# Performance work log

Measured on AMD Instinct MI355X. Metric: run time of the kernel, lower is better.

The kernel has to match this reference:

```python
import jax, jax.numpy as jnp
import numpy as np

K = 20
EPS = 1e-5
NEG_SLOPE = 0.2


def _graph_feature(x, k):
    # x: [B, N, C] -> edge features [B, N, k, 2C]
    xx = jnp.sum(x * x, axis=-1)                       # [B, N]
    inner = jnp.einsum('bnc,bmc->bnm', x, x)           # [B, N, N]
    neg_dist = 2.0 * inner - xx[:, :, None] - xx[:, None, :]
    idx = jax.lax.top_k(neg_dist, k)[1]                # [B, N, k] nearest neighbors
    nbr = jax.vmap(lambda f, i: f[i])(x, idx)          # [B, N, k, C]
    center = jnp.broadcast_to(x[:, :, None, :], nbr.shape)
    return jnp.concatenate([nbr - center, center], axis=-1)


def _bn(y, gamma, beta, axes):
    mu = y.mean(axes, keepdims=True)
    var = y.var(axes, keepdims=True)
    return (y - mu) * jax.lax.rsqrt(var + EPS) * gamma + beta


def _lrelu(y):
    return jnp.where(y > 0, y, NEG_SLOPE * y)


def _edge_block(feat, w, gamma, beta):
    # feat: [B, N, k, Cin], w: [Cout, Cin] (1x1 conv)
    y = jnp.einsum('bnkc,oc->bnko', feat, w)
    y = _lrelu(_bn(y, gamma, beta, (0, 1, 2)))
    return y.max(axis=2)                               # max over k -> [B, N, Cout]


def setup_inputs() -> dict:
    key = jax.random.key(0)
    ks = jax.random.split(key, 8)
    B, N = 16, 2048
    num_features = 128
    x = jax.random.normal(ks[0], (B, N, 3), dtype=jnp.float32)
    s = 0.05
    w1 = jax.random.normal(ks[1], (64, 6), dtype=jnp.float32) * s
    w2 = jax.random.normal(ks[2], (64, 128), dtype=jnp.float32) * s
    w3 = jax.random.normal(ks[3], (128, 128), dtype=jnp.float32) * s
    w4 = jax.random.normal(ks[4], (256, 256), dtype=jnp.float32) * s
    w5 = jax.random.normal(ks[5], (512, 512), dtype=jnp.float32) * s
    we = jax.random.normal(ks[6], (num_features, 512), dtype=jnp.float32) * s
    def gb(c):
        return jnp.ones((c,), jnp.float32), jnp.zeros((c,), jnp.float32)
    g1, b1 = gb(64); g2, b2 = gb(64); g3, b3 = gb(128); g4, b4 = gb(256); g5, b5 = gb(512)
    return dict(x=x, w1=w1, g1=g1, b1=b1, w2=w2, g2=g2, b2=b2, w3=w3, g3=g3, b3=b3,
                w4=w4, g4=g4, b4=b4, w5=w5, g5=g5, b5=b5, we=we)


def reference(x, w1, g1, b1, w2, g2, b2, w3, g3, b3, w4, g4, b4, w5, g5, b5, we):
    # x: [B, N, 3]
    x1 = _edge_block(_graph_feature(x, K), w1, g1, b1)    # [B, N, 64]
    x2 = _edge_block(_graph_feature(x1, K), w2, g2, b2)   # [B, N, 64]
    x3 = _edge_block(_graph_feature(x2, K), w3, g3, b3)   # [B, N, 128]
    x4 = _edge_block(_graph_feature(x3, K), w4, g4, b4)   # [B, N, 256]
    cat = jnp.concatenate([x1, x2, x3, x4], axis=-1)      # [B, N, 512]
    y = jnp.einsum('bnc,oc->bno', cat, w5)                # conv5 (1x1 conv1d)
    y = _lrelu(_bn(y, g5, b5, (0, 1)))
    y = y.max(axis=1)                                     # global max pool -> [B, 512]
    return y @ we.T                                       # embedding -> [B, num_features]
```

## Files before the change

### kernel.cpp

```cpp
#include <hip/hip_runtime.h>
#include <hip/hip_bf16.h>
#include <cstdint>

#define B_ 16
#define N_ 2048
#define KNN_K 20
#define EPS_ 1e-5f
#define SLOPE_ 0.2f
#define IMS 4.8828125e-4f

typedef __attribute__((ext_vector_type(4))) float f32x4;
typedef __attribute__((ext_vector_type(8))) short bf16x8;
typedef __attribute__((ext_vector_type(8))) _Float16 f16x8;

static __device__ __forceinline__ float lrelu(float v){ return v > 0.f ? v : SLOPE_*v; }

static __device__ __forceinline__ unsigned encf(float f){
  unsigned b = __float_as_uint(f);
  return (b & 0x80000000u) ? ~b : (b | 0x80000000u);
}
static __device__ __forceinline__ float decf(unsigned u){
  unsigned b = (u & 0x80000000u) ? (u ^ 0x80000000u) : ~u;
  return __uint_as_float(b);
}
static __device__ __forceinline__ short bfbits(float v){
  __hip_bfloat16 h = __float2bfloat16(v);
  return *reinterpret_cast<short*>(&h);
}
static __device__ __forceinline__ short h16(float v){
  _Float16 h = (_Float16)v;
  return *reinterpret_cast<short*>(&h);
}
static __device__ __forceinline__ float h2f(short s){
  _Float16 h = *reinterpret_cast<_Float16*>(&s);
  return (float)h;
}

template<int C, int CP>
__global__ __launch_bounds__(256) void convert_kernel(const float* __restrict__ f, int lda,
                                                      short* __restrict__ fbf, size_t plane,
                                                      float* __restrict__ xx){
  int wid  = (blockIdx.x * 256 + threadIdx.x) >> 6;
  int lane = threadIdx.x & 63;
  if (wid >= B_*N_) return;
  const float* p = f + (size_t)wid*lda;
  float s = 0.f;
  for (int c = lane; c < CP; c += 64){
    float v = (c < C) ? p[c] : 0.f;
    short h = h16(v);
    short m = h16((v - h2f(h)) * 2048.f);
    size_t o = (size_t)wid*CP + c;
    fbf[o] = h;
    fbf[plane + o] = m;
    s += v*v;
  }
  #pragma unroll
  for (int off=32; off; off>>=1) s += __shfl_down(s, off);
  if (lane==0) xx[wid] = s;
}

template<int CP>
__global__ __launch_bounds__(256, 2) void knn_mfma(const short* __restrict__ fbf, size_t plane,
                                                const float* __restrict__ xx,
                                                float* __restrict__ pval, int* __restrict__ pidx){
  constexpr int SP = CP + 8;
  constexpr int CH = CP/8;
  constexpr int KC = CP/32;
  constexpr int PFH = CP/32;
  constexpr int FMBS = 2*64*SP;
  __shared__ __align__(16) short fmb[FMBS];
  __shared__ float dtile[64*65];
  __shared__ float xn_s[64], xm_s[64];

  int b   = blockIdx.x >> 6;
  int rem = blockIdx.x & 63;
  int n0  = (rem >> 1) << 6;
  int mh  = rem & 1;
  int mbase = mh << 10;
  int tid = threadIdx.x;
  int w    = tid >> 6;
  int lane = tid & 63;
  int fr = lane & 15, hi = lane >> 4;
  int r_loc = lane >> 2, csub = lane & 3;
  int gb = lane & 60;
  int myrow = w*16 + r_loc;
  size_t browoff = (size_t)b * N_;

  f16x8 aH[KC], aM[KC];
  {
    size_t arow = (browoff + n0 + w*16 + fr) * (size_t)CP;
    #pragma unroll
    for (int kc=0; kc<KC; ++kc){
      aH[kc] = *(const f16x8*)&fbf[arow + kc*32 + hi*8];
      aM[kc] = *(const f16x8*)&fbf[plane + arow + kc*32 + hi*8];
    }
  }
  if (tid < 64) xn_s[tid] = xx[browoff + n0 + tid];

  float sv[5]; int si[5];
  #pragma unroll
  for (int j=0;j<5;++j){ sv[j] = -1e30f; si[j] = 0x7FFFFFFF; }

  f16x8 pf[PFH];
  float xmreg = 0.f;
  auto PFLOAD = [&](int mt){
    int m0 = mbase + (mt<<6);
    #pragma unroll
    for (int j=0;j<PFH;++j){
      int i = tid + j*256;
      int r = i/CH, cq = i - r*CH;
      pf[j] = *(const f16x8*)&fbf[(browoff + m0 + r)*(size_t)CP + cq*8];
    }
    if (tid < 64) xmreg = xx[browoff + m0 + tid];
  };
  auto WRITEPF = [&](int mt){
    int m0 = mbase + (mt<<6);
    #pragma unroll
    for (int j=0;j<PFH;++j){
      int i = tid + j*256;
      int r = i/CH, cq = i - r*CH;
      *(f16x8*)&fmb[r*SP + cq*8] = pf[j];
    }
    #pragma unroll
    for (int j=0;j<PFH;++j){
      int i = tid + j*256;
      int r = i/CH, cq = i - r*CH;
      f16x8 v = *(const f16x8*)&fbf[plane + (browoff + m0 + r)*(size_t)CP + cq*8];
      *(f16x8*)&fmb[64*SP + r*SP + cq*8] = v;
    }
    if (tid < 64) xm_s[tid] = xmreg;
  };

  PFLOAD(0);
  WRITEPF(0);
  __syncthreads();

  for (int mt = 0; mt < 16; ++mt){
    int m0 = mbase + (mt << 6);
    if (mt + 1 < 16) PFLOAD(mt + 1);

    f32x4 accH[4], accM[4];
    #pragma unroll
    for (int ct=0; ct<4; ++ct){ accH[ct] = (f32x4){0.f,0.f,0.f,0.f}; accM[ct] = accH[ct]; }
    const short* BH = fmb;
    const short* BM = fmb + 64*SP;
    #pragma unroll
    for (int kc = 0; kc < KC; ++kc){
      #pragma unroll
      for (int ct=0; ct<4; ++ct){
        int boff = (ct*16 + fr)*SP + kc*32 + hi*8;
        f16x8 bh = *(const f16x8*)&BH[boff];
        f16x8 bm = *(const f16x8*)&BM[boff];
        accH[ct] = __builtin_amdgcn_mfma_f32_16x16x32_f16(aH[kc], bh, accH[ct], 0,0,0);
        accM[ct] = __builtin_amdgcn_mfma_f32_16x16x32_f16(aM[kc], bh, accM[ct], 0,0,0);
        accM[ct] = __builtin_amdgcn_mfma_f32_16x16x32_f16(aH[kc], bm, accM[ct], 0,0,0);
      }
    }
    __syncthreads();

    #pragma unroll
    for (int reg=0; reg<4; ++reg){
      int nl = w*16 + hi*4 + reg;
      float xn = xn_s[nl];
      #pragma unroll
      for (int ct=0; ct<4; ++ct)
        dtile[nl*65 + ct*16 + fr] = 2.f*(accH[ct][reg] + IMS*accM[ct][reg]) - xn - xm_s[ct*16 + fr];
    }

    int base = myrow*65 + csub*16;
    float thr = __shfl(sv[4], lane | 3);
    unsigned qm = 0u;
    #pragma unroll
    for (int jj=0; jj<16; ++jj){
      float v = dtile[base + jj];
      qm |= (v > thr) ? (1u << jj) : 0u;
    }
    unsigned long long bal = __ballot(qm != 0u);
    while (bal){
      unsigned nib = (unsigned)((bal >> gb) & 0xFull);
      int leader = nib ? (gb + (int)__builtin_ctz(nib)) : 64;
      int bbit = (int)__builtin_ctz(qm | 0x10000u);
      float mv = dtile[base + (bbit & 15)];
      int mid = m0 + (csub << 4) + bbit;
      float cv = __shfl(mv, leader);
      int   cid = __shfl(mid, leader);
      qm = (lane == leader) ? (qm & (qm - 1u)) : qm;
      int cnt = 0;
      #pragma unroll
      for (int j=0;j<5;++j) cnt += (sv[j] >= cv) ? 1 : 0;
      cnt += __shfl_xor(cnt, 1);
      cnt += __shfl_xor(cnt, 2);
      int pos = nib ? cnt : 20;
      float pv = __shfl_up(sv[4], 1);
      int   pi = __shfl_up(si[4], 1);
      #pragma unroll
      for (int j=0;j<5;++j){
        int g = csub*5 + j;
        float ns = (g < pos) ? sv[j] : ((g == pos) ? cv : pv);
        int   ni = (g < pos) ? si[j] : ((g == pos) ? cid : pi);
        pv = sv[j]; pi = si[j];
        sv[j] = ns; si[j] = ni;
      }
      bal = __ballot(qm != 0u);
    }

    if (mt + 1 < 16){
      WRITEPF(mt + 1);
      __syncthreads();
    }
  }

  size_t orow = browoff + n0 + myrow;
  float* pvo = pval + (orow*2 + mh)*KNN_K + csub*5;
  int*   pio = pidx + (orow*2 + mh)*KNN_K + csub*5;
  #pragma unroll
  for (int j=0;j<5;++j){ pvo[j] = sv[j]; pio[j] = si[j]; }
}

__global__ __launch_bounds__(256) void knn_merge(const float* __restrict__ pval,
                                                 const int* __restrict__ pidx,
                                                 int* __restrict__ idxout){
  int r = blockIdx.x*256 + threadIdx.x;
  if (r >= B_*N_) return;
  const float* va = pval + (size_t)r*2*KNN_K;
  const float* vb = va + KNN_K;
  const int*   ia = pidx + (size_t)r*2*KNN_K;
  const int*   ib = ia + KNN_K;
  int i=0, j=0;
  #pragma unroll
  for (int t=0;t<KNN_K;++t){
    float a = va[i], bq = vb[j];
    bool ta = (a >= bq);
    idxout[(size_t)r*KNN_K + t] = ta ? ia[i] : ib[j];
    i += ta ? 1 : 0; j += ta ? 0 : 1;
  }
}

template<int CP>
__global__ __launch_bounds__(256) void gemm_pq2(const short* __restrict__ fbf, size_t plane,
                                                const float* __restrict__ Wsrc, int Cin,
                                                float* __restrict__ P, float* __restrict__ Qo, int O){
  constexpr int BK = (CP < 64) ? CP : 64;
  constexpr int SP = BK + 8;
  __shared__ short Ah[64*SP];
  __shared__ short Am[64*SP];
  __shared__ short WAh[64*SP];
  __shared__ short WAm[64*SP];
  __shared__ short WQh[64*SP];
  __shared__ short WQm[64*SP];
  int obl = O >> 6;
  int bo = ((int)blockIdx.x % obl) << 6;
  int bm = ((int)blockIdx.x / obl) << 6;
  int tid = threadIdx.x;
  int w = tid >> 6, lane = tid & 63;
  int fr = lane & 15, hi = lane >> 4;
  f32x4 aPH[4], aPM[4], aQH[4], aQM[4];
  #pragma unroll
  for (int ct=0; ct<4; ++ct){
    aPH[ct] = (f32x4){0.f,0.f,0.f,0.f};
    aPM[ct] = aPH[ct]; aQH[ct] = aPH[ct]; aQM[ct] = aPH[ct];
  }

  for (int k0=0; k0<CP; k0+=BK){
    __syncthreads();
    for (int i=tid; i < 64*(BK/8); i += 256){
      int r = i/(BK/8), cq = i%(BK/8);
      size_t src = ((size_t)bm + r)*CP + k0 + cq*8;
      *(f16x8*)&Ah[r*SP + cq*8] = *(const f16x8*)&fbf[src];
      *(f16x8*)&Am[r*SP + cq*8] = *(const f16x8*)&fbf[plane + src];
    }
    for (int i=tid; i < 64*(BK/8); i += 256){
      int r = i/(BK/8), cq = i%(BK/8);
      f16x8 vah, vam, vqh, vqm;
      #pragma unroll
      for (int e=0;e<8;++e){
        int c = k0 + cq*8 + e;
        float wa = 0.f, wqv = 0.f;
        if (c < Cin){
          wa  = Wsrc[(size_t)(bo + r)*2*Cin + c];
          wqv = Wsrc[(size_t)(bo + r)*2*Cin + Cin + c] - wa;
        }
        _Float16 ha = (_Float16)wa;
        vah[e] = ha;
        vam[e] = (_Float16)((wa - (float)ha) * 2048.f);
        _Float16 hq = (_Float16)wqv;
        vqh[e] = hq;
        vqm[e] = (_Float16)((wqv - (float)hq) * 2048.f);
      }
      *(f16x8*)&WAh[r*SP + cq*8] = vah;
      *(f16x8*)&WAm[r*SP + cq*8] = vam;
      *(f16x8*)&WQh[r*SP + cq*8] = vqh;
      *(f16x8*)&WQm[r*SP + cq*8] = vqm;
    }
    __syncthreads();
    #pragma unroll
    for (int kc=0; kc<BK/32; ++kc){
      f16x8 ah = *(const f16x8*)&Ah[(w*16 + fr)*SP + kc*32 + hi*8];
      f16x8 am = *(const f16x8*)&Am[(w*16 + fr)*SP + kc*32 + hi*8];
      #pragma unroll
      for (int ct=0; ct<4; ++ct){
        int boff = (ct*16 + fr)*SP + kc*32 + hi*8;
        f16x8 bh = *(const f16x8*)&WAh[boff];
        f16x8 bm = *(const f16x8*)&WAm[boff];
        f16x8 qh = *(const f16x8*)&WQh[boff];
        f16x8 qm = *(const f16x8*)&WQm[boff];
        aPH[ct] = __builtin_amdgcn_mfma_f32_16x16x32_f16(ah, bh, aPH[ct], 0,0,0);
        aPM[ct] = __builtin_amdgcn_mfma_f32_16x16x32_f16(am, bh, aPM[ct], 0,0,0);
        aPM[ct] = __builtin_amdgcn_mfma_f32_16x16x32_f16(ah, bm, aPM[ct], 0,0,0);
        aQH[ct] = __builtin_amdgcn_mfma_f32_16x16x32_f16(ah, qh, aQH[ct], 0,0,0);
        aQM[ct] = __builtin_amdgcn_mfma_f32_16x16x32_f16(am, qh, aQM[ct], 0,0,0);
        aQM[ct] = __builtin_amdgcn_mfma_f32_16x16x32_f16(ah, qm, aQM[ct], 0,0,0);
      }
    }
  }
  #pragma unroll
  for (int ct=0; ct<4; ++ct)
    #pragma unroll
    for (int reg=0; reg<4; ++reg){
      int row = bm + w*16 + hi*4 + reg;
      size_t o = (size_t)row*O + bo + ct*16 + fr;
      P[o]  = aPH[ct][reg] + IMS*aPM[ct][reg];
      Qo[o] = aQH[ct][reg] + IMS*aQM[ct][reg];
    }
}

__global__ __launch_bounds__(256) void gemm_bf16_stats(const float* __restrict__ A,
                                                       const float* __restrict__ Wt,
                                                       const float* __restrict__ g5,
                                                       float* __restrict__ sums,
                                                       float* __restrict__ sumsq,
                                                       unsigned* __restrict__ maxenc){
  __shared__ short As[128*72];
  __shared__ short Bs[64*72];
  __shared__ float s1[64], s2[64];
  int bm = (int)(blockIdx.x >> 3) << 7;
  int bo = (int)(blockIdx.x & 7) << 6;
  int tid = threadIdx.x;
  int w = tid >> 6, lane = tid & 63;
  int fr = lane & 15, hi = lane >> 4;
  f32x4 acc[2][4];
  #pragma unroll
  for (int g=0; g<2; ++g)
    #pragma unroll
    for (int ct=0; ct<4; ++ct) acc[g][ct] = (f32x4){0.f,0.f,0.f,0.f};

  for (int k0=0; k0<512; k0+=64){
    __syncthreads();
    #pragma unroll 2
    for (int i = tid; i < 1024; i += 256){
      int r = i >> 3, cq = i & 7;
      const float* src = &A[(size_t)(bm + r)*512 + k0 + cq*8];
      bf16x8 v;
      #pragma unroll
      for (int e=0;e<8;++e) v[e] = bfbits(src[e]);
      *(bf16x8*)&As[r*72 + cq*8] = v;
    }
    #pragma unroll 2
    for (int i = tid; i < 512; i += 256){
      int r = i >> 3, cq = i & 7;
      const float* src = &Wt[(size_t)(bo + r)*512 + k0 + cq*8];
      bf16x8 v;
      #pragma unroll
      for (int e=0;e<8;++e) v[e] = bfbits(src[e]);
      *(bf16x8*)&Bs[r*72 + cq*8] = v;
    }
    __syncthreads();
    #pragma unroll
    for (int kc=0; kc<2; ++kc){
      bf16x8 a0 = *(const bf16x8*)&As[(w*32 +      fr)*72 + kc*32 + hi*8];
      bf16x8 a1 = *(const bf16x8*)&As[(w*32 + 16 + fr)*72 + kc*32 + hi*8];
      #pragma unroll
      for (int ct=0; ct<4; ++ct){
        bf16x8 bb = *(const bf16x8*)&Bs[(ct*16 + fr)*72 + kc*32 + hi*8];
        acc[0][ct] = __builtin_amdgcn_mfma_f32_16x16x32_bf16(a0, bb, acc[0][ct], 0,0,0);
        acc[1][ct] = __builtin_amdgcn_mfma_f32_16x16x32_bf16(a1, bb, acc[1][ct], 0,0,0);
      }
    }
  }

  __syncthreads();
  if (tid < 64){ s1[tid] = 0.f; s2[tid] = 0.f; }
  __syncthreads();
  int bidx = bm >> 11;
  #pragma unroll
  for (int ct=0; ct<4; ++ct){
    int o = bo + ct*16 + fr;
    float ga = g5[o];
    float s = 0.f, ss = 0.f, mx = -1e30f;
    #pragma unroll
    for (int g=0; g<2; ++g)
      #pragma unroll
      for (int reg=0; reg<4; ++reg){
        float v = acc[g][ct][reg];
        s += v; ss += v*v;
        float sel = ga >= 0.f ? v : -v;
        mx = fmaxf(mx, sel);
      }
    s  += __shfl_xor(s, 16);  s  += __shfl_xor(s, 32);
    ss += __shfl_xor(ss, 16); ss += __shfl_xor(ss, 32);
    mx = fmaxf(mx, __shfl_xor(mx, 16)); mx = fmaxf(mx, __shfl_xor(mx, 32));
    if (hi == 0){
      atomicAdd(&s1[ct*16 + fr], s);
      atomicAdd(&s2[ct*16 + fr], ss);
      atomicMax(&maxenc[bidx*512 + o], encf(mx));
    }
  }
  __syncthreads();
  if (tid < 64){
    atomicAdd(&sums[bo + tid],  s1[tid]);
    atomicAdd(&sumsq[bo + tid], s2[tid]);
  }
}

__global__ void zero_f_kernel(float* p, int n){
  int i = blockIdx.x*blockDim.x + threadIdx.x;
  if (i < n) p[i] = 0.f;
}
__global__ void zero_u_kernel(unsigned* p, int n){
  int i = blockIdx.x*blockDim.x + threadIdx.x;
  if (i < n) p[i] = 0u;
}

__global__ __launch_bounds__(256) void edge_agg(const float* __restrict__ P, const float* __restrict__ Q,
      const int* __restrict__ idx, const float* __restrict__ gamma,
      float* __restrict__ S, float* __restrict__ sums, float* __restrict__ sumsq, int O){
  const int ROWS = 64;
  int rpi = 256 / O;
  int iters = ROWS / rpi;
  int row0 = blockIdx.x * ROWS;
  int tid = threadIdx.x;
  int o  = tid % O;
  int rl = tid / O;
  int b  = row0 / N_;
  __shared__ int sidx[4][KNN_K];
  __shared__ float s1[256], s2[256];
  float g = gamma[o];
  float csum=0.f, csumsq=0.f;
  for (int it=0; it<iters; ++it){
    __syncthreads();
    if (tid < KNN_K*rpi) sidx[tid/KNN_K][tid%KNN_K] = idx[(size_t)(row0 + it*rpi)*KNN_K + tid];
    __syncthreads();
    int row = row0 + it*rpi + rl;
    float q = Q[(size_t)row*O + o];
    float mx=-1e30f, mn=1e30f, s=0.f, ss=0.f;
    #pragma unroll
    for (int k=0;k<KNN_K;++k){
      int m = sidx[rl][k];
      float p = P[((size_t)b*N_ + m)*O + o];
      mx = fmaxf(mx,p); mn = fminf(mn,p);
      float y = p + q; s += y; ss += y*y;
    }
    csum += s; csumsq += ss;
    S[(size_t)row*O + o] = (g >= 0.f ? mx : mn) + q;
  }
  s1[tid]=0.f; s2[tid]=0.f;
  __syncthreads();
  atomicAdd(&s1[o], csum); atomicAdd(&s2[o], csumsq);
  __syncthreads();
  if (tid < O){ atomicAdd(&sums[tid], s1[tid]); atomicAdd(&sumsq[tid], s2[tid]); }
}

__global__ void bn_finalize(const float* __restrict__ sums, const float* __restrict__ sumsq,
                            const float* __restrict__ gamma, const float* __restrict__ beta,
                            float invM, float* __restrict__ scale, float* __restrict__ shift, int O){
  int o = blockIdx.x*blockDim.x + threadIdx.x;
  if (o >= O) return;
  float mu = sums[o]*invM;
  float var = sumsq[o]*invM - mu*mu;
  float rs = rsqrtf(var + EPS_);
  float sc = gamma[o]*rs;
  scale[o] = sc; shift[o] = beta[o] - mu*sc;
}

__global__ void apply_write(const float* __restrict__ S, const float* __restrict__ scale,
                            const float* __restrict__ shift, float* __restrict__ cat, int off, int O){
  int i = blockIdx.x*blockDim.x + threadIdx.x;
  if (i >= B_*N_*O) return;
  int row = i / O, o = i - row*O;
  float v = S[i]*scale[o] + shift[o];
  cat[(size_t)row*512 + off + o] = lrelu(v);
}

__global__ void pool_kernel(const unsigned* __restrict__ maxenc, const float* __restrict__ scale,
                            const float* __restrict__ shift, const float* __restrict__ g5,
                            float* __restrict__ pooled){
  int i = blockIdx.x*blockDim.x + threadIdx.x;
  if (i >= B_*512) return;
  int o = i & 511;
  float t = decf(maxenc[i]);
  float y = g5[o] >= 0.f ? t : -t;
  pooled[i] = lrelu(y*scale[o] + shift[o]);
}

__global__ void final_mm(const float* __restrict__ pooled, const float* __restrict__ we,
                         float* __restrict__ out){
  int i = blockIdx.x*blockDim.x + threadIdx.x;
  if (i >= B_*128) return;
  int b = i >> 7, j = i & 127;
  const float4* pp = (const float4*)(pooled + (size_t)b*512);
  const float4* wp = (const float4*)(we + (size_t)j*512);
  float s = 0.f;
  for (int c=0;c<128;++c){
    float4 a = pp[c], w = wp[c];
    s += a.x*w.x + a.y*w.y + a.z*w.z + a.w*w.w;
  }
  out[i] = s;
}

struct Ws {
  float* cat; float* P; float* Q; float* S; int* idx; float* xx;
  float* sums; float* sumsq; float* scale; float* shift;
  unsigned* maxenc; float* pooled; short* fbf;
  float* pval; int* pidx;
};

template<int C, int CP>
static void run_layer(const Ws& W, const float* f, int lda, int O,
                      const float* w, const float* g, const float* bt,
                      int off_out, hipStream_t stream){
  const int M = B_*N_;
  size_t plane = (size_t)M*CP;
  convert_kernel<C, CP><<<M/4, 256, 0, stream>>>(f, lda, W.fbf, plane, W.xx);
  knn_mfma<CP><<<B_*(N_/64)*2, 256, 0, stream>>>(W.fbf, plane, W.xx, W.pval, W.pidx);
  knn_merge<<<(M+255)/256, 256, 0, stream>>>(W.pval, W.pidx, W.idx);
  int grid = (M/64)*(O/64);
  gemm_pq2<CP><<<grid, 256, 0, stream>>>(W.fbf, plane, w, C, W.P, W.Q, O);
  zero_f_kernel<<<4, 256, 0, stream>>>(W.sums, 1024);
  edge_agg<<<M/64, 256, 0, stream>>>(W.P, W.Q, W.idx, g, W.S, W.sums, W.sumsq, O);
  bn_finalize<<<(O+255)/256, 256, 0, stream>>>(W.sums, W.sumsq, g, bt,
                                               1.f/((float)M*KNN_K), W.scale, W.shift, O);
  apply_write<<<(M*O+255)/256, 256, 0, stream>>>(W.S, W.scale, W.shift, W.cat, off_out, O);
}

extern "C" void kernel_launch(void* const* d_in, const int* in_sizes, int n_in,
                              void* d_out, int out_size, void* d_ws, size_t ws_size,
                              hipStream_t stream) {
  const float* x  = (const float*)d_in[0];
  const float* w1 = (const float*)d_in[1];
  const float* g1 = (const float*)d_in[2];
  const float* b1 = (const float*)d_in[3];
  const float* w2 = (const float*)d_in[4];
  const float* g2 = (const float*)d_in[5];
  const float* b2 = (const float*)d_in[6];
  const float* w3 = (const float*)d_in[7];
  const float* g3 = (const float*)d_in[8];
  const float* b3 = (const float*)d_in[9];
  const float* w4 = (const float*)d_in[10];
  const float* g4 = (const float*)d_in[11];
  const float* b4 = (const float*)d_in[12];
  const float* w5 = (const float*)d_in[13];
  const float* g5 = (const float*)d_in[14];
  const float* b5 = (const float*)d_in[15];
  const float* we = (const float*)d_in[16];

  char* ws = (char*)d_ws;
  Ws W;
  size_t off = 0;
  W.cat   = (float*)(ws + off); off += (size_t)16*2048*512*4;
  W.P     = (float*)(ws + off); off += (size_t)16*2048*256*4;
  W.Q     = (float*)(ws + off); off += (size_t)16*2048*256*4;
  char* R = ws + off;            off += (size_t)16*2048*256*4;
  W.idx   = (int*)  (ws + off); off += (size_t)16*2048*20*4;
  W.xx    = (float*)(ws + off); off += (size_t)16*2048*4;
  W.sums  = (float*)(ws + off); off += 512*4;
  W.sumsq = (float*)(ws + off); off += 512*4;
  W.scale = (float*)(ws + off); off += 512*4;
  W.shift = (float*)(ws + off); off += 512*4;
  W.maxenc= (unsigned*)(ws + off); off += (size_t)16*512*4;
  W.pooled= (float*)(ws + off); off += (size_t)16*512*4;
  W.S     = (float*)R;
  W.fbf   = (short*)R;
  W.pval  = W.Q;
  W.pidx  = (int*)(W.Q + (size_t)2*16*2048*KNN_K);

  const int M = B_*N_;

  run_layer<3,   32>(W, x,           3,   64,  w1, g1, b1, 0,   stream);
  run_layer<64,  64>(W, W.cat,       512, 64,  w2, g2, b2, 64,  stream);
  run_layer<64,  64>(W, W.cat + 64,  512, 128, w3, g3, b3, 128, stream);
  run_layer<128,128>(W, W.cat + 128, 512, 256, w4, g4, b4, 256, stream);

  zero_f_kernel<<<4, 256, 0, stream>>>(W.sums, 1024);
  zero_u_kernel<<<32, 256, 0, stream>>>(W.maxenc, 16*512);
  gemm_bf16_stats<<<(M/128)*8, 256, 0, stream>>>(W.cat, w5, g5, W.sums, W.sumsq, W.maxenc);
  bn_finalize<<<2, 256, 0, stream>>>(W.sums, W.sumsq, g5, b5, 1.f/(float)M, W.scale, W.shift, 512);
  pool_kernel<<<(16*512+255)/256, 256, 0, stream>>>(W.maxenc, W.scale, W.shift, g5, W.pooled);
  final_mm<<<(16*128+255)/256, 256, 0, stream>>>(W.pooled, we, (float*)d_out);
}
```

Before: 1.156 ms.

## Raise kNN occupancy by dropping register prefetch and row-constant distance term

The kNN MFMA kernel now targets three blocks per SM instead of two. To fit, it drops the register-held prefetch buffer and loads the next candidate tile straight into shared memory after the distance tile is written, so the load overlaps the top-k selection phase. The MFMA loop is reordered to finish one 16-column slice at a time, so only one pair of accumulators is live. The per-row |x_n|^2 term is removed because it does not change the ranking within a row, which saves a shared array and some arithmetic. The risk is that global-load latency is now exposed inside the loop rather than hidden in registers, and the stored partial values are shifted by a per-row constant that the merge step must tolerate.

```diff
diff --git a/kernel.cpp b/kernel.cpp
--- a/kernel.cpp
+++ b/kernel.cpp
@@ -60,17 +60,16 @@
 }
 
 template<int CP>
-__global__ __launch_bounds__(256, 2) void knn_mfma(const short* __restrict__ fbf, size_t plane,
+__global__ __launch_bounds__(256, 3) void knn_mfma(const short* __restrict__ fbf, size_t plane,
                                                 const float* __restrict__ xx,
                                                 float* __restrict__ pval, int* __restrict__ pidx){
   constexpr int SP = CP + 8;
   constexpr int CH = CP/8;
   constexpr int KC = CP/32;
   constexpr int PFH = CP/32;
-  constexpr int FMBS = 2*64*SP;
-  __shared__ __align__(16) short fmb[FMBS];
+  __shared__ __align__(16) short fmb[2*64*SP];
   __shared__ float dtile[64*65];
-  __shared__ float xn_s[64], xm_s[64];
+  __shared__ float xm_s[64];
 
   int b   = blockIdx.x >> 6;
   int rem = blockIdx.x & 63;
@@ -95,77 +94,53 @@
       aM[kc] = *(const f16x8*)&fbf[plane + arow + kc*32 + hi*8];
     }
   }
-  if (tid < 64) xn_s[tid] = xx[browoff + n0 + tid];
 
   float sv[5]; int si[5];
   #pragma unroll
   for (int j=0;j<5;++j){ sv[j] = -1e30f; si[j] = 0x7FFFFFFF; }
 
-  f16x8 pf[PFH];
-  float xmreg = 0.f;
-  auto PFLOAD = [&](int mt){
+  auto STAGE = [&](int mt){
     int m0 = mbase + (mt<<6);
     #pragma unroll
     for (int j=0;j<PFH;++j){
       int i = tid + j*256;
       int r = i/CH, cq = i - r*CH;
-      pf[j] = *(const f16x8*)&fbf[(browoff + m0 + r)*(size_t)CP + cq*8];
-    }
-    if (tid < 64) xmreg = xx[browoff + m0 + tid];
+      size_t src = (browoff + m0 + r)*(size_t)CP + cq*8;
+      *(f16x8*)&fmb[r*SP + cq*8] = *(const f16x8*)&fbf[src];
+      *(f16x8*)&fmb[64*SP + r*SP + cq*8] = *(const f16x8*)&fbf[plane + src];
+    }
+    if (tid < 64) xm_s[tid] = xx[browoff + m0 + tid];
   };
-  auto WRITEPF = [&](int mt){
-    int m0 = mbase + (mt<<6);
-    #pragma unroll
-    for (int j=0;j<PFH;++j){
-      int i = tid + j*256;
-      int r = i/CH, cq = i - r*CH;
-      *(f16x8*)&fmb[r*SP + cq*8] = pf[j];
-    }
-    #pragma unroll
-    for (int j=0;j<PFH;++j){
-      int i = tid + j*256;
-      int r = i/CH, cq = i - r*CH;
-      f16x8 v = *(const f16x8*)&fbf[plane + (browoff + m0 + r)*(size_t)CP + cq*8];
-      *(f16x8*)&fmb[64*SP + r*SP + cq*8] = v;
-    }
-    if (tid < 64) xm_s[tid] = xmreg;
-  };
-
-  PFLOAD(0);
-  WRITEPF(0);
+
+  STAGE(0);
   __syncthreads();
 
   for (int mt = 0; mt < 16; ++mt){
     int m0 = mbase + (mt << 6);
-    if (mt + 1 < 16) PFLOAD(mt + 1);
-
-    f32x4 accH[4], accM[4];
-    #pragma unroll
-    for (int ct=0; ct<4; ++ct){ accH[ct] = (f32x4){0.f,0.f,0.f,0.f}; accM[ct] = accH[ct]; }
-    const short* BH = fmb;
-    const short* BM = fmb + 64*SP;
-    #pragma unroll
-    for (int kc = 0; kc < KC; ++kc){
-      #pragma unroll
-      for (int ct=0; ct<4; ++ct){
+
+    #pragma unroll
+    for (int ct=0; ct<4; ++ct){
+      f32x4 accH = (f32x4){0.f,0.f,0.f,0.f};
+      f32x4 accM = accH;
+      #pragma unroll
+      for (int kc=0; kc<KC; ++kc){
         int boff = (ct*16 + fr)*SP + kc*32 + hi*8;
-        f16x8 bh = *(const f16x8*)&BH[boff];
-        f16x8 bm = *(const f16x8*)&BM[boff];
-        accH[ct] = __builtin_amdgcn_mfma_f32_16x16x32_f16(aH[kc], bh, accH[ct], 0,0,0);
-        accM[ct] = __builtin_amdgcn_mfma_f32_16x16x32_f16(aM[kc], bh, accM[ct], 0,0,0);
-        accM[ct] = __builtin_amdgcn_mfma_f32_16x16x32_f16(aH[kc], bm, accM[ct], 0,0,0);
-      }
-    }
-    __syncthreads();
-
-    #pragma unroll
-    for (int reg=0; reg<4; ++reg){
-      int nl = w*16 + hi*4 + reg;
-      float xn = xn_s[nl];
-      #pragma unroll
-      for (int ct=0; ct<4; ++ct)
-        dtile[nl*65 + ct*16 + fr] = 2.f*(accH[ct][reg] + IMS*accM[ct][reg]) - xn - xm_s[ct*16 + fr];
-    }
+        f16x8 bh = *(const f16x8*)&fmb[boff];
+        f16x8 bm = *(const f16x8*)&fmb[64*SP + boff];
+        accH = __builtin_amdgcn_mfma_f32_16x16x32_f16(aH[kc], bh, accH, 0,0,0);
+        accM = __builtin_amdgcn_mfma_f32_16x16x32_f16(aM[kc], bh, accM, 0,0,0);
+        accM = __builtin_amdgcn_mfma_f32_16x16x32_f16(aH[kc], bm, accM, 0,0,0);
+      }
+      float xm = xm_s[ct*16 + fr];
+      #pragma unroll
+      for (int reg=0; reg<4; ++reg){
+        int nl = w*16 + hi*4 + reg;
+        dtile[nl*65 + ct*16 + fr] = 2.f*(accH[reg] + IMS*accM[reg]) - xm;
+      }
+    }
+    __syncthreads();
+
+    if (mt + 1 < 16) STAGE(mt + 1);
 
     int base = myrow*65 + csub*16;
     float thr = __shfl(sv[4], lane | 3);
@@ -204,10 +179,7 @@
       bal = __ballot(qm != 0u);
     }
 
-    if (mt + 1 < 16){
-      WRITEPF(mt + 1);
-      __syncthreads();
-    }
+    if (mt + 1 < 16) __syncthreads();
   }
 
   size_t orow = browoff + n0 + myrow;
```

Result: no change. 1.147 ms, median of 2 (-0.8%).
